# Kernel tuning notes

Hardware: AMD Instinct MI355X
Metric: run time of the kernel (lower is better)

## Reference

```python
import jax, jax.numpy as jnp
import numpy as np

N, E, G, M = 65536, 262144, 1024, 64   # nodes, edges, graphs, max nodes/graph
D, H, C, ED, P, L = 512, 8, 64, 128, 1024, 5  # hidden, heads, head_dim, edge_dim, proj_dim, layers
SLOPE = 0.2  # PyG GATv2 leaky_relu negative slope


def rmsnorm(x, w):
    eps = jnp.asarray(jnp.finfo(x.dtype).eps, x.dtype)
    return x * jax.lax.rsqrt(jnp.mean(x * x, axis=-1, keepdims=True) + eps) * w


def gat_layer(x, src, dst, eattr, Wl, bl, Wr, br, We, att, gb):
    # GATv2Conv(concat=True, edge_dim, add_self_loops=False), eval mode
    xl = (x @ Wl + bl).reshape(N, H, C)
    xr = (x @ Wr + br).reshape(N, H, C)
    ee = (eattr @ We).reshape(E, H, C)
    s = xl[src] + xr[dst] + ee                      # [E,H,C]
    s = jnp.where(s > 0, s, SLOPE * s)              # leaky_relu
    logits = jnp.einsum('ehc,hc->eh', s, att)       # [E,H]
    mx = jax.ops.segment_max(logits, dst, num_segments=N)
    p = jnp.exp(logits - mx[dst])
    denom = jax.ops.segment_sum(p, dst, num_segments=N)
    alpha = p / denom[dst]                          # segment softmax over in-edges of dst
    msg = xl[src] * alpha[:, :, None]               # [E,H,C]
    return jax.ops.segment_sum(msg, dst, num_segments=N).reshape(N, H * C) + gb


def setup_inputs():
    key = jax.random.key(0)
    ks = jax.random.split(key, 32)
    f = lambda k, shp: 0.02 * jax.random.normal(k, shp, dtype=jnp.float32)
    inp = {}
    inp['node_x'] = jax.random.randint(ks[0], (N, 9), 0, 2, dtype=jnp.int32)
    inp['edge_attr_idx'] = jax.random.randint(ks[1], (E, 3), 0, 2, dtype=jnp.int32)
    inp['edge_index'] = jax.random.randint(ks[2], (2, E), 0, N, dtype=jnp.int32)
    inp['batch'] = jnp.arange(N, dtype=jnp.int32) // M  # sorted graph ids, 64 atoms/graph
    # MolEncoder embedding tables, padded to max vocab (indices stay in-range)
    inp['atom_emb'] = f(ks[3], (9, 119, D))
    inp['edge_emb'] = f(ks[4], (3, 22, ED))
    # 5 GATv2Block layers, params stacked on leading axis
    inp['Wl'] = f(ks[5], (L, D, D)); inp['bl'] = f(ks[6], (L, D))
    inp['Wr'] = f(ks[7], (L, D, D)); inp['br'] = f(ks[8], (L, D))
    inp['We'] = f(ks[9], (L, ED, D))
    inp['att'] = f(ks[10], (L, H, C))
    inp['gb'] = f(ks[11], (L, D))
    inp['n1w'] = jnp.ones((L, D), jnp.float32)
    inp['f1w'] = f(ks[12], (L, D, 4 * D)); inp['f1b'] = f(ks[13], (L, 4 * D))
    inp['f2w'] = f(ks[14], (L, 4 * D, D)); inp['f2b'] = f(ks[15], (L, D))
    inp['n2w'] = jnp.ones((L, D), jnp.float32)
    # attention pooling + projection head
    inp['gapW'] = f(ks[16], (D, D)); inp['gapb'] = f(ks[17], (D,))
    inp['avW'] = f(ks[18], (D,)); inp['avb'] = f(ks[19], (1,))
    inp['p1W'] = f(ks[20], (D, P)); inp['p1b'] = f(ks[21], (P,))
    inp['pnw'] = jnp.ones((P,), jnp.float32)
    inp['p2W'] = f(ks[22], (P, P)); inp['p2b'] = f(ks[23], (P,))
    return inp


def reference(node_x, edge_attr_idx, edge_index, batch, atom_emb, edge_emb, Wl, bl, Wr, br, We, att, gb, n1w, f1w, f1b, f2w, f2b, n2w, gapW, gapb, avW, avb, p1W, p1b, pnw, p2W, p2b):
    src, dst = edge_index[0], edge_index[1]
    # MolEncoder: sum of categorical embeddings
    x = atom_emb[jnp.arange(9)[None, :], node_x].sum(axis=1)              # [N,D]
    eattr = edge_emb[jnp.arange(3)[None, :], edge_attr_idx].sum(axis=1)   # [E,ED]
    for l in range(L):
        xa = gat_layer(x, src, dst, eattr, Wl[l], bl[l], Wr[l], br[l], We[l], att[l], gb[l])
        x = rmsnorm(x + xa, n1w[l])
        h = jax.nn.gelu(x @ f1w[l] + f1b[l], approximate=False) @ f2w[l] + f2b[l]
        x = rmsnorm(x + h, n2w[l])
    # to_dense_batch with static max_nodes = M
    counts = jax.ops.segment_sum(jnp.ones(N, jnp.int32), batch, num_segments=G)
    starts = jnp.concatenate([jnp.zeros(1, jnp.int32), jnp.cumsum(counts)[:-1].astype(jnp.int32)])
    pos = jnp.arange(N, dtype=jnp.int32) - starts[batch]
    x_dense = jnp.zeros((G, M, D), x.dtype).at[batch, pos].set(x)
    mask = jnp.zeros((G, M), bool).at[batch, pos].set(True)
    # graph attention pooling
    z = x_dense @ gapW + gapb                                             # [G,M,D]
    a = (z @ avW + avb[0])[:, :, None]                                    # [G,M,1]
    a = jnp.where(mask[:, :, None], a, -jnp.inf)
    alpha = jax.nn.softmax(a, axis=1)
    h_graph = jnp.sum(z * alpha, axis=1)                                  # [G,D]
    hp = jax.nn.relu(rmsnorm(h_graph @ p1W + p1b, pnw))
    z_graph_pool = hp @ p2W + p2b                                         # [G,P]
    return z_graph_pool, x_dense, mask
```

## Files before the change

kernel.cpp:

```cpp
#include <hip/hip_runtime.h>
#include <hip/hip_bf16.h>
#include <math.h>

namespace {

using bf16 = __hip_bfloat16;
typedef __bf16 bf16x8 __attribute__((ext_vector_type(8)));
typedef float f32x4 __attribute__((ext_vector_type(4)));

constexpr int N_ = 65536, E_ = 262144, G_ = 1024, M_ = 64;
constexpr int D_ = 512, H_ = 8, C_ = 64, ED_ = 128, P_ = 1024, L_ = 5;
constexpr float SLOPE = 0.2f;
constexpr float EPSF = 1.1920929e-7f;

constexpr int NCH = 2;
constexpr int NCHUNK = N_ / NCH;

constexpr int TV = 22;
constexpr int TK = TV * TV * TV;
constexpr int TKP = 10752;

__device__ inline float b2f(bf16 h) { return __bfloat162float(h); }
__device__ inline bf16 f2b(float f) { return __float2bfloat16(f); }
__device__ inline float us2f(unsigned short u) {
  return __uint_as_float((unsigned)u << 16);
}
__device__ inline unsigned short f2us(float f) {
  bf16 b = __float2bfloat16(f);
  return *(unsigned short*)&b;
}

typedef __attribute__((address_space(1))) void as1_void_t;
typedef __attribute__((address_space(3))) void as3_void_t;
__device__ inline void gload16(const void* g, void* l) {
  __builtin_amdgcn_global_load_lds((const as1_void_t*)g, (as3_void_t*)l, 16, 0,
                                   0);
}

template <int EPI, int OBF>
__global__ __launch_bounds__(256) void mfma_gemm_k(
    const ushort* __restrict__ A, const ushort* __restrict__ Bt,
    const float* __restrict__ bias, void* __restrict__ Cv, int M, int K,
    int Nc) {
  __shared__ __align__(16) ushort As[128 * 64];
  __shared__ __align__(16) ushort Bs[128 * 64];
  const int tid = threadIdx.x;
  const int wave = tid >> 6, lane = tid & 63;
  const int m0 = blockIdx.x * 128, n0 = blockIdx.y * 128;
  const int wr = wave >> 1, wc = wave & 1;
  const int srow = tid >> 3;
  const int skoff = (((tid & 7) ^ (srow & 7)) << 3);
  const ushort* Ap = A + (size_t)(m0 + srow) * K + skoff;
  const ushort* Bp = Bt + (size_t)(n0 + srow) * K + skoff;
  char* AsB = (char*)As + wave * 1024;
  char* BsB = (char*)Bs + wave * 1024;
  const int fr = lane & 15, fg = lane >> 4;
  const int rx = fr & 7;
  const int sA0 = ((fg) ^ rx) << 3;
  const int sA1 = ((4 | fg) ^ rx) << 3;
  const ushort* Arow = As + (wr * 64 + fr) * 64;
  const ushort* Brow = Bs + (wc * 64 + fr) * 64;
  f32x4 acc[4][4];
#pragma unroll
  for (int i = 0; i < 4; ++i)
#pragma unroll
    for (int j = 0; j < 4; ++j) acc[i][j] = (f32x4){0.f, 0.f, 0.f, 0.f};

  for (int kt = 0; kt < K; kt += 64) {
#pragma unroll
    for (int r = 0; r < 4; ++r) {
      gload16(Ap + kt + (size_t)r * 32 * K, AsB + r * 4096);
      gload16(Bp + kt + (size_t)r * 32 * K, BsB + r * 4096);
    }
    __syncthreads();
    bf16x8 af[4], bg[4];
#pragma unroll
    for (int i = 0; i < 4; ++i)
      af[i] = *(const bf16x8*)(Arow + i * 1024 + sA0);
#pragma unroll
    for (int j = 0; j < 4; ++j)
      bg[j] = *(const bf16x8*)(Brow + j * 1024 + sA0);
#pragma unroll
    for (int i = 0; i < 4; ++i)
#pragma unroll
      for (int j = 0; j < 4; ++j)
        acc[i][j] = __builtin_amdgcn_mfma_f32_16x16x32_bf16(af[i], bg[j],
                                                            acc[i][j], 0, 0, 0);
#pragma unroll
    for (int i = 0; i < 4; ++i)
      af[i] = *(const bf16x8*)(Arow + i * 1024 + sA1);
#pragma unroll
    for (int j = 0; j < 4; ++j)
      bg[j] = *(const bf16x8*)(Brow + j * 1024 + sA1);
#pragma unroll
    for (int i = 0; i < 4; ++i)
#pragma unroll
      for (int j = 0; j < 4; ++j)
        acc[i][j] = __builtin_amdgcn_mfma_f32_16x16x32_bf16(af[i], bg[j],
                                                            acc[i][j], 0, 0, 0);
    __syncthreads();
  }
  const int cb = n0 + wc * 64 + fr;
  float bv[4];
#pragma unroll
  for (int j = 0; j < 4; ++j) bv[j] = bias ? bias[cb + j * 16] : 0.f;
#pragma unroll
  for (int i = 0; i < 4; ++i) {
#pragma unroll
    for (int r = 0; r < 4; ++r) {
      int m = m0 + wr * 64 + i * 16 + fg * 4 + r;
      size_t rb = (size_t)m * Nc + cb;
#pragma unroll
      for (int j = 0; j < 4; ++j) {
        float c = acc[i][j][r] + bv[j];
        if (EPI == 1) c = 0.5f * c * (1.f + erff(c * 0.70710678118654752f));
        if (OBF)
          ((bf16*)Cv)[rb + j * 16] = f2b(c);
        else
          ((float*)Cv)[rb + j * 16] = c;
      }
    }
  }
}

__global__ __launch_bounds__(256) void transpose_cvt_k(
    const float* __restrict__ W, bf16* __restrict__ Wt, int K, int N) {
  __shared__ float tile[32][33];
  int bn = blockIdx.x * 32, bk = blockIdx.y * 32;
  int tx = threadIdx.x, ty = threadIdx.y;
#pragma unroll
  for (int i = ty; i < 32; i += 8) tile[i][tx] = W[(size_t)(bk + i) * N + bn + tx];
  __syncthreads();
#pragma unroll
  for (int i = ty; i < 32; i += 8)
    Wt[(size_t)(bn + i) * K + bk + tx] = f2b(tile[tx][i]);
}

template <int EPI, typename TIN, typename TOUT>
__global__ __launch_bounds__(256) void gemm_bias_k(
    const TIN* __restrict__ A, const float* __restrict__ B,
    const float* __restrict__ bias, TOUT* __restrict__ C, int M, int K,
    int Nc) {
  __shared__ float As[64][17];
  __shared__ float Bs[16][68];
  const int tid = threadIdx.x;
  const int m0 = blockIdx.x * 64;
  const int n0 = blockIdx.y * 64;
  const int ty = tid >> 4, tx = tid & 15;
  const int lam = tid >> 2;
  const int lak = (tid & 3) << 2;
  const int lbk = tid >> 4;
  const int lbn = (tid & 15) << 2;
  const TIN* Aptr = A + (long)(m0 + lam) * K + lak;
  const float* Bptr = B + (long)lbk * Nc + n0 + lbn;
  float acc[4][4] = {};
  for (int kt = 0; kt < K; kt += 16) {
    float4 va = *(const float4*)(Aptr + kt);
    float4 vb = *(const float4*)(Bptr + (long)kt * Nc);
    __syncthreads();
    As[lam][lak + 0] = va.x; As[lam][lak + 1] = va.y;
    As[lam][lak + 2] = va.z; As[lam][lak + 3] = va.w;
    Bs[lbk][lbn + 0] = vb.x; Bs[lbk][lbn + 1] = vb.y;
    Bs[lbk][lbn + 2] = vb.z; Bs[lbk][lbn + 3] = vb.w;
    __syncthreads();
#pragma unroll
    for (int kk = 0; kk < 16; ++kk) {
      float a[4], b[4];
#pragma unroll
      for (int i = 0; i < 4; ++i) a[i] = As[ty * 4 + i][kk];
#pragma unroll
      for (int j = 0; j < 4; ++j) b[j] = Bs[kk][tx * 4 + j];
#pragma unroll
      for (int i = 0; i < 4; ++i)
#pragma unroll
        for (int j = 0; j < 4; ++j) acc[i][j] = fmaf(a[i], b[j], acc[i][j]);
    }
  }
#pragma unroll
  for (int i = 0; i < 4; ++i) {
    long row = (long)(m0 + ty * 4 + i) * Nc + n0;
#pragma unroll
    for (int j = 0; j < 4; ++j) {
      float c = acc[i][j] + (bias ? bias[n0 + tx * 4 + j] : 0.f);
      if (EPI == 1) c = 0.5f * c * (1.f + erff(c * 0.70710678118654752f));
      ((float*)C)[row + tx * 4 + j] = c;
    }
  }
}

__global__ __launch_bounds__(256) void encode_nodes_k(
    const int* __restrict__ nodeX, const float* __restrict__ atomEmb,
    bf16* __restrict__ x) {
  int n = blockIdx.x, tid = threadIdx.x;
  __shared__ int idx[9];
  if (tid < 9) idx[tid] = nodeX[n * 9 + tid];
  __syncthreads();
  for (int d = tid; d < D_; d += 256) {
    float s = 0.f;
#pragma unroll
    for (int k = 0; k < 9; ++k) s += atomEmb[(k * 119 + idx[k]) * D_ + d];
    x[(long)n * D_ + d] = f2b(s);
  }
}

__global__ __launch_bounds__(256) void build_keys_k(
    const int* __restrict__ eai, int* __restrict__ keys) {
  int e = blockIdx.x * 256 + threadIdx.x;
  keys[e] = eai[e * 3] * (TV * TV) + eai[e * 3 + 1] * TV + eai[e * 3 + 2];
}

__global__ __launch_bounds__(128) void build_eattr_tab_k(
    const float* __restrict__ edgeEmb, bf16* __restrict__ tab) {
  int r = blockIdx.x, d = threadIdx.x;
  float s = 0.f;
  if (r < TK) {
    int k0 = r / (TV * TV), k1 = (r / TV) % TV, k2 = r % TV;
    s = edgeEmb[(0 * TV + k0) * ED_ + d] + edgeEmb[(1 * TV + k1) * ED_ + d] +
        edgeEmb[(2 * TV + k2) * ED_ + d];
  }
  tab[(size_t)r * ED_ + d] = f2b(s);
}

__global__ __launch_bounds__(256) void edge_logits_k(
    const ushort* __restrict__ xl, const ushort* __restrict__ xr,
    const ushort* __restrict__ ee_tab, const int* __restrict__ keys,
    const float* __restrict__ att, const int* __restrict__ src,
    const int* __restrict__ dst, float* __restrict__ logits) {
  int e = blockIdx.x * 4 + (threadIdx.x >> 6);
  int lane = threadIdx.x & 63;
  int s = src[e], t = dst[e], key = keys[e];
  int d0 = lane * 8;
  uint4 a = *(const uint4*)(xl + (size_t)s * D_ + d0);
  uint4 b = *(const uint4*)(xr + (size_t)t * D_ + d0);
  uint4 c = *(const uint4*)(ee_tab + (size_t)key * D_ + d0);
  float p = 0.f;
#pragma unroll
  for (int w = 0; w < 4; ++w) {
    unsigned ua = (&a.x)[w], ub = (&b.x)[w], uc = (&c.x)[w];
    float v0 = us2f((ushort)ua) + us2f((ushort)ub) + us2f((ushort)uc);
    float v1 = us2f((ushort)(ua >> 16)) + us2f((ushort)(ub >> 16)) +
               us2f((ushort)(uc >> 16));
    v0 = (v0 > 0.f) ? v0 : SLOPE * v0;
    v1 = (v1 > 0.f) ? v1 : SLOPE * v1;
    p = fmaf(v0, att[d0 + 2 * w], p);
    p = fmaf(v1, att[d0 + 2 * w + 1], p);
  }
#pragma unroll
  for (int o = 1; o < 8; o <<= 1) p += __shfl_xor(p, o);
  if ((lane & 7) == 0) {
    logits[(size_t)e * H_ + (lane >> 3)] = p;
  }
}

__global__ __launch_bounds__(256) void gat_aggr_norm_k(
    bf16* __restrict__ x, const bf16* __restrict__ xl,
    const float* __restrict__ logits, const int* __restrict__ ptr,
    const int* __restrict__ eid, const int* __restrict__ src,
    const float* __restrict__ gb, const float* __restrict__ w) {
  constexpr int PCAP = 40;
  __shared__ int se_e[PCAP], se_s[PCAP];
  __shared__ float pa[PCAP * 8];
  __shared__ float mh[8], invden[8];
  __shared__ float wsum[4];
  int n = blockIdx.x, tid = threadIdx.x;
  int beg = ptr[n], deg = ptr[n + 1] - beg;
  if (tid < PCAP && tid < deg) {
    int ed = eid[beg + tid];
    se_e[tid] = ed;
    se_s[tid] = src[ed];
  }
  __syncthreads();
  if (tid < 8) {
    int h = tid;
    float m = -__builtin_inff();
    for (int i = 0; i < deg; ++i) {
      int e = (i < PCAP) ? se_e[i] : eid[beg + i];
      m = fmaxf(m, logits[(size_t)e * H_ + h]);
    }
    float den = 0.f;
    for (int i = 0; i < deg; ++i) {
      int e = (i < PCAP) ? se_e[i] : eid[beg + i];
      float p = expf(logits[(size_t)e * H_ + h] - m);
      den += p;
      if (i < PCAP) pa[i * 8 + h] = p;
    }
    mh[h] = m;
    invden[h] = (deg > 0) ? 1.f / den : 0.f;
  }
  __syncthreads();
  int h = tid >> 5;
  float acc0 = 0.f, acc1 = 0.f;
  for (int i = 0; i < deg; ++i) {
    float p;
    int s;
    if (i < PCAP) {
      p = pa[i * 8 + h];
      s = se_s[i];
    } else {
      int e = eid[beg + i];
      s = src[e];
      p = expf(logits[(size_t)e * H_ + h] - mh[h]);
    }
    unsigned u = *(const unsigned*)((const ushort*)xl + (size_t)s * D_ + tid * 2);
    acc0 = fmaf(us2f((ushort)u), p, acc0);
    acc1 = fmaf(us2f((ushort)(u >> 16)), p, acc1);
  }
  float inv = invden[h];
  long base = (long)n * D_;
  unsigned xu = *(const unsigned*)((const ushort*)x + base + tid * 2);
  float v0 = us2f((ushort)xu) + acc0 * inv + gb[tid * 2];
  float v1 = us2f((ushort)(xu >> 16)) + acc1 * inv + gb[tid * 2 + 1];
  float ss = v0 * v0 + v1 * v1;
#pragma unroll
  for (int o = 32; o > 0; o >>= 1) ss += __shfl_xor(ss, o);
  if ((tid & 63) == 0) wsum[tid >> 6] = ss;
  __syncthreads();
  float tot = wsum[0] + wsum[1] + wsum[2] + wsum[3];
  float scale = rsqrtf(tot * (1.0f / D_) + EPSF);
  unsigned outw = (unsigned)f2us(v0 * scale * w[tid * 2]) |
                  ((unsigned)f2us(v1 * scale * w[tid * 2 + 1]) << 16);
  *(unsigned*)((ushort*)x + base + tid * 2) = outw;
}

__global__ __launch_bounds__(256) void rmsnorm_res_k(
    bf16* __restrict__ x, const float* __restrict__ xa,
    const float* __restrict__ w) {
  int n = blockIdx.x, tid = threadIdx.x;
  long base = (long)n * D_;
  float v0 = b2f(x[base + tid]) + xa[base + tid];
  float v1 = b2f(x[base + tid + 256]) + xa[base + tid + 256];
  float ss = v0 * v0 + v1 * v1;
#pragma unroll
  for (int o = 32; o > 0; o >>= 1) ss += __shfl_xor(ss, o);
  __shared__ float wsum[4];
  if ((tid & 63) == 0) wsum[tid >> 6] = ss;
  __syncthreads();
  float tot = wsum[0] + wsum[1] + wsum[2] + wsum[3];
  float scale = rsqrtf(tot * (1.0f / D_) + EPSF);
  x[base + tid] = f2b(v0 * scale * w[tid]);
  x[base + tid + 256] = f2b(v1 * scale * w[tid + 256]);
}

__global__ void zero_int_k(int* __restrict__ p) {
  p[blockIdx.x * 256 + threadIdx.x] = 0;
}
__global__ void count_k(const int* __restrict__ key, int* __restrict__ counts) {
  int id = blockIdx.x * 256 + threadIdx.x;
  atomicAdd(&counts[key[id]], 1);
}
__global__ void copy_int_k(const int* __restrict__ in, int* __restrict__ out) {
  int id = blockIdx.x * 256 + threadIdx.x;
  out[id] = in[id];
}
__global__ void fill_csr_k(const int* __restrict__ dst,
                           int* __restrict__ cursor, int* __restrict__ eid) {
  int e = blockIdx.x * 256 + threadIdx.x;
  int pos = atomicAdd(&cursor[dst[e]], 1);
  eid[pos] = e;
}
__global__ __launch_bounds__(1024) void scanN_k(const int* __restrict__ cnt,
                                                int* __restrict__ ptr) {
  __shared__ int sums[1024];
  int t = threadIdx.x;
  int base = t * 64;
  int s = 0;
  for (int i = 0; i < 64; ++i) s += cnt[base + i];
  sums[t] = s;
  __syncthreads();
  for (int off = 1; off < 1024; off <<= 1) {
    int v = (t >= off) ? sums[t - off] : 0;
    __syncthreads();
    sums[t] += v;
    __syncthreads();
  }
  int run = (t > 0) ? sums[t - 1] : 0;
  for (int i = 0; i < 64; ++i) {
    ptr[base + i] = run;
    run += cnt[base + i];
  }
  if (t == 1023) ptr[N_] = run;
}
__global__ void scan_k(const int* __restrict__ counts, int* __restrict__ starts) {
  __shared__ int buf[G_];
  int t = threadIdx.x;
  int c = counts[t];
  buf[t] = c;
  __syncthreads();
  for (int off = 1; off < G_; off <<= 1) {
    int v = (t >= off) ? buf[t - off] : 0;
    __syncthreads();
    buf[t] += v;
    __syncthreads();
  }
  starts[t] = buf[t] - c;
}

__global__ __launch_bounds__(256) void pool_k(
    const bf16* __restrict__ z, const float* __restrict__ avW,
    const float* __restrict__ avb, const int* __restrict__ counts,
    const int* __restrict__ starts, float* __restrict__ hg) {
  int g = blockIdx.x, tid = threadIdx.x;
  int cnt = counts[g], st = starts[g];
  __shared__ float aL[M_];
  int wave = tid >> 6, lane = tid & 63;
  for (int m = wave; m < M_; m += 4) {
    float s = 0.f;
    if (m < cnt) {
      const bf16* row = z + (long)(st + m) * D_;
      for (int c = lane; c < D_; c += 64) s += b2f(row[c]) * avW[c];
    }
#pragma unroll
    for (int o = 32; o > 0; o >>= 1) s += __shfl_xor(s, o);
    if (lane == 0) aL[m] = s;
  }
  __syncthreads();
  if (tid < 64) {
    float v = (tid < cnt) ? aL[tid] + avb[0] : -__builtin_inff();
    float mxv = v;
#pragma unroll
    for (int o = 32; o > 0; o >>= 1) mxv = fmaxf(mxv, __shfl_xor(mxv, o));
    float p = (tid < cnt) ? expf(v - mxv) : 0.f;
    float sm = p;
#pragma unroll
    for (int o = 32; o > 0; o >>= 1) sm += __shfl_xor(sm, o);
    aL[tid] = p / sm;
  }
  __syncthreads();
  for (int d = tid; d < D_; d += 256) {
    float acc = 0.f;
    for (int m = 0; m < cnt; ++m) acc += b2f(z[(long)(st + m) * D_ + d]) * aL[m];
    hg[(long)g * D_ + d] = acc;
  }
}

__global__ __launch_bounds__(256) void rms_relu_k(
    const float* __restrict__ in, const float* __restrict__ w,
    float* __restrict__ out) {
  int g = blockIdx.x, tid = threadIdx.x;
  long base = (long)g * P_;
  float v[4], ss = 0.f;
#pragma unroll
  for (int k = 0; k < 4; ++k) {
    v[k] = in[base + tid + k * 256];
    ss += v[k] * v[k];
  }
#pragma unroll
  for (int o = 32; o > 0; o >>= 1) ss += __shfl_xor(ss, o);
  __shared__ float wsum[4];
  if ((tid & 63) == 0) wsum[tid >> 6] = ss;
  __syncthreads();
  float tot = wsum[0] + wsum[1] + wsum[2] + wsum[3];
  float scale = rsqrtf(tot * (1.0f / P_) + EPSF);
#pragma unroll
  for (int k = 0; k < 4; ++k) {
    float c = v[k] * scale * w[tid + k * 256];
    out[base + tid + k * 256] = fmaxf(c, 0.f);
  }
}

__global__ __launch_bounds__(256) void write_dense_k(
    const bf16* __restrict__ x, const int* __restrict__ counts,
    const int* __restrict__ starts, float* __restrict__ out1) {
  long id = (long)blockIdx.x * 256 + threadIdx.x;
  int g = (int)(id >> 15);
  int rem = (int)(id & 32767);
  int m = rem >> 9, d = rem & 511;
  float v = 0.f;
  if (m < counts[g]) v = b2f(x[(long)(starts[g] + m) * D_ + d]);
  out1[id] = v;
}
__global__ void write_mask_k(const int* __restrict__ counts,
                             float* __restrict__ out2) {
  int id = blockIdx.x * 256 + threadIdx.x;
  out2[id] = ((id & 63) < counts[id >> 6]) ? 1.f : 0.f;
}

}

extern "C" void kernel_launch(void* const* d_in, const int* in_sizes, int n_in,
                              void* d_out, int out_size, void* d_ws,
                              size_t ws_size, hipStream_t stream) {
  const int* node_x = (const int*)d_in[0];
  const int* edge_attr_idx = (const int*)d_in[1];
  const int* edge_index = (const int*)d_in[2];
  const int* batch = (const int*)d_in[3];
  const float* atom_emb = (const float*)d_in[4];
  const float* edge_emb = (const float*)d_in[5];
  const float* Wl = (const float*)d_in[6];
  const float* bl = (const float*)d_in[7];
  const float* Wr = (const float*)d_in[8];
  const float* br = (const float*)d_in[9];
  const float* We = (const float*)d_in[10];
  const float* att = (const float*)d_in[11];
  const float* gb = (const float*)d_in[12];
  const float* n1w = (const float*)d_in[13];
  const float* f1w = (const float*)d_in[14];
  const float* f1b = (const float*)d_in[15];
  const float* f2w = (const float*)d_in[16];
  const float* f2b = (const float*)d_in[17];
  const float* n2w = (const float*)d_in[18];
  const float* gapW = (const float*)d_in[19];
  const float* gapb = (const float*)d_in[20];
  const float* avW = (const float*)d_in[21];
  const float* avb = (const float*)d_in[22];
  const float* p1W = (const float*)d_in[23];
  const float* p1b = (const float*)d_in[24];
  const float* pnw = (const float*)d_in[25];
  const float* p2W = (const float*)d_in[26];
  const float* p2b = (const float*)d_in[27];
  const int* src = edge_index;
  const int* dst = edge_index + E_;

  char* ws = (char*)d_ws;
  bf16* x = (bf16*)ws;
  bf16* xl = x + (long)N_ * D_;
  bf16* xr = xl + (long)N_ * D_;
  bf16* region = xr + (long)N_ * D_;
  bf16* ee_tab = region;
  bf16* eattr_tab = ee_tab + (long)TKP * D_;
  float* logits = (float*)(region + (long)32768 * D_ + (long)32768 * ED_);
  int* keys = (int*)(logits + (long)E_ * H_);
  float* denom_unused = (float*)(keys + N_ * H_);
  int* counts = (int*)(denom_unused + (long)N_ * H_);
  int* starts = counts + G_;
  float* hg = (float*)(starts + G_);
  float* tmpP = hg + (long)G_ * D_;
  float* hp = tmpP + (long)G_ * P_;
  bf16* hid = xl;

  bf16* wsc = (bf16*)tmpP;
  bf16* Wl_b = wsc;
  bf16* Wr_b = Wl_b + 512 * 512;
  bf16* We_b = Wr_b + 512 * 512;
  bf16* f1w_b = We_b + 512 * 128;
  bf16* f2w_b = f1w_b + 2048 * 512;

  float* out0 = (float*)d_out;
  float* out1 = out0 + (long)G_ * P_;
  float* out2 = out1 + (long)G_ * M_ * D_;
  float* xa = out1;

  int* csr_eid = (int*)out0;
  int* csr_ptr = csr_eid + E_;
  int* cursor = csr_ptr + N_ + 1;

  encode_nodes_k<<<N_, 256, 0, stream>>>(node_x, atom_emb, x);

  build_keys_k<<<E_ / 256, 256, 0, stream>>>(edge_attr_idx, keys);
  build_eattr_tab_k<<<TKP, 128, 0, stream>>>(edge_emb, eattr_tab);
  zero_int_k<<<N_ / 256, 256, 0, stream>>>(cursor);
  count_k<<<E_ / 256, 256, 0, stream>>>(dst, cursor);
  scanN_k<<<1, 1024, 0, stream>>>(cursor, csr_ptr);
  copy_int_k<<<N_ / 256, 256, 0, stream>>>(csr_ptr, cursor);
  fill_csr_k<<<E_ / 256, 256, 0, stream>>>(dst, cursor, csr_eid);

  for (int l = 0; l < L_; ++l) {
    const float* Wl_l = Wl + (long)l * D_ * D_;
    const float* bl_l = bl + (long)l * D_;
    const float* Wr_l = Wr + (long)l * D_ * D_;
    const float* br_l = br + (long)l * D_;
    const float* We_l = We + (long)l * ED_ * D_;
    const float* att_l = att + (long)l * H_ * C_;
    const float* gb_l = gb + (long)l * D_;
    const float* n1w_l = n1w + (long)l * D_;
    const float* f1w_l = f1w + (long)l * D_ * 4 * D_;
    const float* f1b_l = f1b + (long)l * 4 * D_;
    const float* f2w_l = f2w + (long)l * 4 * D_ * D_;
    const float* f2b_l = f2b + (long)l * D_;
    const float* n2w_l = n2w + (long)l * D_;

    transpose_cvt_k<<<dim3(16, 16), dim3(32, 8), 0, stream>>>(Wl_l, Wl_b, 512, 512);
    transpose_cvt_k<<<dim3(16, 16), dim3(32, 8), 0, stream>>>(Wr_l, Wr_b, 512, 512);
    transpose_cvt_k<<<dim3(16, 4), dim3(32, 8), 0, stream>>>(We_l, We_b, 128, 512);
    transpose_cvt_k<<<dim3(64, 16), dim3(32, 8), 0, stream>>>(f1w_l, f1w_b, 512, 2048);
    transpose_cvt_k<<<dim3(16, 64), dim3(32, 8), 0, stream>>>(f2w_l, f2w_b, 2048, 512);

    mfma_gemm_k<0, 1><<<dim3(N_ / 128, D_ / 128), 256, 0, stream>>>(
        (const ushort*)x, (const ushort*)Wl_b, bl_l, xl, N_, D_, D_);
    mfma_gemm_k<0, 1><<<dim3(N_ / 128, D_ / 128), 256, 0, stream>>>(
        (const ushort*)x, (const ushort*)Wr_b, br_l, xr, N_, D_, D_);
    mfma_gemm_k<0, 1><<<dim3(TKP / 128, D_ / 128), 256, 0, stream>>>(
        (const ushort*)eattr_tab, (const ushort*)We_b, nullptr, ee_tab, TKP,
        ED_, D_);
    edge_logits_k<<<E_ / 4, 256, 0, stream>>>(
        (const ushort*)xl, (const ushort*)xr, (const ushort*)ee_tab, keys,
        att_l, src, dst, logits);
    gat_aggr_norm_k<<<N_, 256, 0, stream>>>(x, xl, logits, csr_ptr, csr_eid,
                                            src, gb_l, n1w_l);

    for (int nc = 0; nc < NCH; ++nc) {
      long nbase = (long)nc * NCHUNK;
      mfma_gemm_k<1, 1><<<dim3(NCHUNK / 128, (4 * D_) / 128), 256, 0, stream>>>(
          (const ushort*)(x + nbase * D_), (const ushort*)f1w_b, f1b_l, hid,
          NCHUNK, D_, 4 * D_);
      mfma_gemm_k<0, 0><<<dim3(NCHUNK / 128, D_ / 128), 256, 0, stream>>>(
          (const ushort*)hid, (const ushort*)f2w_b, f2b_l, xa + nbase * D_,
          NCHUNK, 4 * D_, D_);
    }
    rmsnorm_res_k<<<N_, 256, 0, stream>>>(x, xa, n2w_l);
  }

  zero_int_k<<<G_ / 256, 256, 0, stream>>>(counts);
  count_k<<<N_ / 256, 256, 0, stream>>>(batch, counts);
  scan_k<<<1, G_, 0, stream>>>(counts, starts);

  bf16* gapW_b = eattr_tab;
  transpose_cvt_k<<<dim3(16, 16), dim3(32, 8), 0, stream>>>(gapW, gapW_b, 512, 512);
  mfma_gemm_k<0, 1><<<dim3(N_ / 128, D_ / 128), 256, 0, stream>>>(
      (const ushort*)x, (const ushort*)gapW_b, gapb, xl, N_, D_, D_);
  pool_k<<<G_, 256, 0, stream>>>(xl, avW, avb, counts, starts, hg);
  gemm_bias_k<0, float, float><<<dim3(G_ / 64, P_ / 64), 256, 0, stream>>>(
      hg, p1W, p1b, tmpP, G_, D_, P_);
  rms_relu_k<<<G_, 256, 0, stream>>>(tmpP, pnw, hp);
  gemm_bias_k<0, float, float><<<dim3(G_ / 64, P_ / 64), 256, 0, stream>>>(
      hp, p2W, p2b, out0, G_, P_, P_);

  write_dense_k<<<(int)(((long)G_ * M_ * D_) / 256), 256, 0, stream>>>(
      x, counts, starts, out1);
  write_mask_k<<<(G_ * M_) / 256, 256, 0, stream>>>(counts, out2);
}
```

Measured before the change: 5.131 ms.

## Fuse GATv2 edge logits, online segment softmax, aggregation and rmsnorm per node

Replaces the separate edge-logit kernel and the per-node aggregation kernel with one kernel that assigns one wavefront per destination node. The kernel computes logits on the fly from xl, xr and the edge table, and applies an online softmax with running max rescaling in chunks of four edges. It then accumulates messages and applies the residual rmsnorm. This removes the logits buffer round trip and the second gather of xl rows, and raises the work per thread from two to eight channels. In exchange, edge work is grouped by destination degree, which may cause load imbalance and serialized chunk latency within a wave.

Result: faster. 4.118 ms (-19.7%).

```diff
diff --git a/kernel.cpp b/kernel.cpp
--- a/kernel.cpp
+++ b/kernel.cpp
@@ -19,6 +19,8 @@
 constexpr int TV = 22;
 constexpr int TK = TV * TV * TV;
 constexpr int TKP = 10752;
+
+constexpr int CH = 4;
 
 __device__ inline float b2f(bf16 h) { return __bfloat162float(h); }
 __device__ inline bf16 f2b(float f) { return __float2bfloat16(f); }
@@ -221,105 +223,123 @@
   tab[(size_t)r * ED_ + d] = f2b(s);
 }
 
-__global__ __launch_bounds__(256) void edge_logits_k(
-    const ushort* __restrict__ xl, const ushort* __restrict__ xr,
-    const ushort* __restrict__ ee_tab, const int* __restrict__ keys,
-    const float* __restrict__ att, const int* __restrict__ src,
-    const int* __restrict__ dst, float* __restrict__ logits) {
-  int e = blockIdx.x * 4 + (threadIdx.x >> 6);
-  int lane = threadIdx.x & 63;
-  int s = src[e], t = dst[e], key = keys[e];
-  int d0 = lane * 8;
-  uint4 a = *(const uint4*)(xl + (size_t)s * D_ + d0);
-  uint4 b = *(const uint4*)(xr + (size_t)t * D_ + d0);
-  uint4 c = *(const uint4*)(ee_tab + (size_t)key * D_ + d0);
-  float p = 0.f;
-#pragma unroll
-  for (int w = 0; w < 4; ++w) {
-    unsigned ua = (&a.x)[w], ub = (&b.x)[w], uc = (&c.x)[w];
-    float v0 = us2f((ushort)ua) + us2f((ushort)ub) + us2f((ushort)uc);
-    float v1 = us2f((ushort)(ua >> 16)) + us2f((ushort)(ub >> 16)) +
-               us2f((ushort)(uc >> 16));
-    v0 = (v0 > 0.f) ? v0 : SLOPE * v0;
-    v1 = (v1 > 0.f) ? v1 : SLOPE * v1;
-    p = fmaf(v0, att[d0 + 2 * w], p);
-    p = fmaf(v1, att[d0 + 2 * w + 1], p);
-  }
-#pragma unroll
-  for (int o = 1; o < 8; o <<= 1) p += __shfl_xor(p, o);
-  if ((lane & 7) == 0) {
-    logits[(size_t)e * H_ + (lane >> 3)] = p;
-  }
-}
-
-__global__ __launch_bounds__(256) void gat_aggr_norm_k(
-    bf16* __restrict__ x, const bf16* __restrict__ xl,
-    const float* __restrict__ logits, const int* __restrict__ ptr,
-    const int* __restrict__ eid, const int* __restrict__ src,
-    const float* __restrict__ gb, const float* __restrict__ w) {
-  constexpr int PCAP = 40;
-  __shared__ int se_e[PCAP], se_s[PCAP];
-  __shared__ float pa[PCAP * 8];
-  __shared__ float mh[8], invden[8];
-  __shared__ float wsum[4];
-  int n = blockIdx.x, tid = threadIdx.x;
-  int beg = ptr[n], deg = ptr[n + 1] - beg;
-  if (tid < PCAP && tid < deg) {
-    int ed = eid[beg + tid];
-    se_e[tid] = ed;
-    se_s[tid] = src[ed];
-  }
-  __syncthreads();
-  if (tid < 8) {
-    int h = tid;
-    float m = -__builtin_inff();
-    for (int i = 0; i < deg; ++i) {
-      int e = (i < PCAP) ? se_e[i] : eid[beg + i];
-      m = fmaxf(m, logits[(size_t)e * H_ + h]);
-    }
-    float den = 0.f;
-    for (int i = 0; i < deg; ++i) {
-      int e = (i < PCAP) ? se_e[i] : eid[beg + i];
-      float p = expf(logits[(size_t)e * H_ + h] - m);
-      den += p;
-      if (i < PCAP) pa[i * 8 + h] = p;
-    }
-    mh[h] = m;
-    invden[h] = (deg > 0) ? 1.f / den : 0.f;
-  }
-  __syncthreads();
-  int h = tid >> 5;
-  float acc0 = 0.f, acc1 = 0.f;
-  for (int i = 0; i < deg; ++i) {
-    float p;
-    int s;
-    if (i < PCAP) {
-      p = pa[i * 8 + h];
-      s = se_s[i];
-    } else {
-      int e = eid[beg + i];
-      s = src[e];
-      p = expf(logits[(size_t)e * H_ + h] - mh[h]);
-    }
-    unsigned u = *(const unsigned*)((const ushort*)xl + (size_t)s * D_ + tid * 2);
-    acc0 = fmaf(us2f((ushort)u), p, acc0);
-    acc1 = fmaf(us2f((ushort)(u >> 16)), p, acc1);
-  }
-  float inv = invden[h];
-  long base = (long)n * D_;
-  unsigned xu = *(const unsigned*)((const ushort*)x + base + tid * 2);
-  float v0 = us2f((ushort)xu) + acc0 * inv + gb[tid * 2];
-  float v1 = us2f((ushort)(xu >> 16)) + acc1 * inv + gb[tid * 2 + 1];
-  float ss = v0 * v0 + v1 * v1;
-#pragma unroll
-  for (int o = 32; o > 0; o >>= 1) ss += __shfl_xor(ss, o);
-  if ((tid & 63) == 0) wsum[tid >> 6] = ss;
-  __syncthreads();
-  float tot = wsum[0] + wsum[1] + wsum[2] + wsum[3];
-  float scale = rsqrtf(tot * (1.0f / D_) + EPSF);
-  unsigned outw = (unsigned)f2us(v0 * scale * w[tid * 2]) |
-                  ((unsigned)f2us(v1 * scale * w[tid * 2 + 1]) << 16);
-  *(unsigned*)((ushort*)x + base + tid * 2) = outw;
+__global__ __launch_bounds__(256) void gat_fused_k(
+    bf16* __restrict__ x, const ushort* __restrict__ xl,
+    const ushort* __restrict__ xr, const ushort* __restrict__ ee_tab,
+    const int* __restrict__ keys, const float* __restrict__ att,
+    const int* __restrict__ ptr, const int* __restrict__ eid,
+    const int* __restrict__ src, const float* __restrict__ gb,
+    const float* __restrict__ w) {
+  const int wave = threadIdx.x >> 6, lane = threadIdx.x & 63;
+  const int n = blockIdx.x * 4 + wave;
+  const int d0 = lane * 8;
+  const int beg = ptr[n], deg = ptr[n + 1] - beg;
+
+  float4 a0 = *(const float4*)(att + d0);
+  float4 a1 = *(const float4*)(att + d0 + 4);
+  float attv[8] = {a0.x, a0.y, a0.z, a0.w, a1.x, a1.y, a1.z, a1.w};
+  uint4 xru = *(const uint4*)(xr + (size_t)n * D_ + d0);
+  float xrf[8];
+#pragma unroll
+  for (int q = 0; q < 4; ++q) {
+    unsigned u = (&xru.x)[q];
+    xrf[2 * q] = us2f((ushort)u);
+    xrf[2 * q + 1] = us2f((ushort)(u >> 16));
+  }
+
+  float m = -__builtin_inff(), den = 0.f;
+  float acc[8] = {0.f, 0.f, 0.f, 0.f, 0.f, 0.f, 0.f, 0.f};
+
+  for (int c0 = 0; c0 < deg; c0 += CH) {
+    int cn = min(deg - c0, CH);
+    int s_l = 0, k_l = 0;
+    if (lane < cn) {
+      int e = eid[beg + c0 + lane];
+      s_l = src[e];
+      k_l = keys[e];
+    }
+    uint4 xlv[CH];
+    float lg[CH];
+#pragma unroll
+    for (int i = 0; i < CH; ++i) {
+      lg[i] = -__builtin_inff();
+      if (i < cn) {
+        int s = __shfl(s_l, i);
+        int k = __shfl(k_l, i);
+        xlv[i] = *(const uint4*)(xl + (size_t)s * D_ + d0);
+        uint4 ev = *(const uint4*)(ee_tab + (size_t)k * D_ + d0);
+        float part = 0.f;
+#pragma unroll
+        for (int q = 0; q < 4; ++q) {
+          unsigned ua = (&xlv[i].x)[q];
+          unsigned ue = (&ev.x)[q];
+          float v0 = us2f((ushort)ua) + xrf[2 * q] + us2f((ushort)ue);
+          float v1 =
+              us2f((ushort)(ua >> 16)) + xrf[2 * q + 1] + us2f((ushort)(ue >> 16));
+          v0 = (v0 > 0.f) ? v0 : SLOPE * v0;
+          v1 = (v1 > 0.f) ? v1 : SLOPE * v1;
+          part = fmaf(v0, attv[2 * q], part);
+          part = fmaf(v1, attv[2 * q + 1], part);
+        }
+        part += __shfl_xor(part, 1);
+        part += __shfl_xor(part, 2);
+        part += __shfl_xor(part, 4);
+        lg[i] = part;
+      }
+    }
+    float cm = lg[0];
+#pragma unroll
+    for (int i = 1; i < CH; ++i) cm = fmaxf(cm, lg[i]);
+    if (cm > m) {
+      float sc = expf(m - cm);
+      den *= sc;
+#pragma unroll
+      for (int j = 0; j < 8; ++j) acc[j] *= sc;
+      m = cm;
+    }
+#pragma unroll
+    for (int i = 0; i < CH; ++i) {
+      if (i < cn) {
+        float p = expf(lg[i] - m);
+        den += p;
+#pragma unroll
+        for (int q = 0; q < 4; ++q) {
+          unsigned ua = (&xlv[i].x)[q];
+          acc[2 * q] = fmaf(us2f((ushort)ua), p, acc[2 * q]);
+          acc[2 * q + 1] = fmaf(us2f((ushort)(ua >> 16)), p, acc[2 * q + 1]);
+        }
+      }
+    }
+  }
+
+  float inv = (deg > 0) ? 1.f / den : 0.f;
+  uint4 xu = *(const uint4*)((const ushort*)x + (size_t)n * D_ + d0);
+  float4 g0 = *(const float4*)(gb + d0);
+  float4 g1 = *(const float4*)(gb + d0 + 4);
+  float gbv[8] = {g0.x, g0.y, g0.z, g0.w, g1.x, g1.y, g1.z, g1.w};
+  float v[8], ss = 0.f;
+#pragma unroll
+  for (int q = 0; q < 4; ++q) {
+    unsigned u = (&xu.x)[q];
+    v[2 * q] = us2f((ushort)u) + acc[2 * q] * inv + gbv[2 * q];
+    v[2 * q + 1] = us2f((ushort)(u >> 16)) + acc[2 * q + 1] * inv + gbv[2 * q + 1];
+  }
+#pragma unroll
+  for (int j = 0; j < 8; ++j) ss += v[j] * v[j];
+#pragma unroll
+  for (int o = 1; o < 64; o <<= 1) ss += __shfl_xor(ss, o);
+  float scale = rsqrtf(ss * (1.0f / D_) + EPSF);
+  float4 w0 = *(const float4*)(w + d0);
+  float4 w1 = *(const float4*)(w + d0 + 4);
+  float wv[8] = {w0.x, w0.y, w0.z, w0.w, w1.x, w1.y, w1.z, w1.w};
+  uint4 outv;
+#pragma unroll
+  for (int q = 0; q < 4; ++q) {
+    unsigned lo = f2us(v[2 * q] * scale * wv[2 * q]);
+    unsigned hi = f2us(v[2 * q + 1] * scale * wv[2 * q + 1]);
+    (&outv.x)[q] = lo | (hi << 16);
+  }
+  *(uint4*)((ushort*)x + (size_t)n * D_ + d0) = outv;
 }
 
 __global__ __launch_bounds__(256) void rmsnorm_res_k(
@@ -518,8 +538,8 @@
   bf16* region = xr + (long)N_ * D_;
   bf16* ee_tab = region;
   bf16* eattr_tab = ee_tab + (long)TKP * D_;
-  float* logits = (float*)(region + (long)32768 * D_ + (long)32768 * ED_);
-  int* keys = (int*)(logits + (long)E_ * H_);
+  float* logits_unused = (float*)(region + (long)32768 * D_ + (long)32768 * ED_);
+  int* keys = (int*)(logits_unused + (long)E_ * H_);
   float* denom_unused = (float*)(keys + N_ * H_);
   int* counts = (int*)(denom_unused + (long)N_ * H_);
   int* starts = counts + G_;
@@ -582,11 +602,10 @@
     mfma_gemm_k<0, 1><<<dim3(TKP / 128, D_ / 128), 256, 0, stream>>>(
         (const ushort*)eattr_tab, (const ushort*)We_b, nullptr, ee_tab, TKP,
         ED_, D_);
-    edge_logits_k<<<E_ / 4, 256, 0, stream>>>(
-        (const ushort*)xl, (const ushort*)xr, (const ushort*)ee_tab, keys,
-        att_l, src, dst, logits);
-    gat_aggr_norm_k<<<N_, 256, 0, stream>>>(x, xl, logits, csr_ptr, csr_eid,
-                                            src, gb_l, n1w_l);
+
+    gat_fused_k<<<N_ / 4, 256, 0, stream>>>(
+        x, (const ushort*)xl, (const ushort*)xr, (const ushort*)ee_tab, keys,
+        att_l, csr_ptr, csr_eid, src, gb_l, n1w_l);
 
     for (int nc = 0; nc < NCH; ++nc) {
       long nbase = (long)nc * NCHUNK;
```
